# Performance work log

Hardware: AMD Instinct MI355X
Metric: run time of the kernel (lower is better)

## Reference

```python
import jax, jax.numpy as jnp
import numpy as np

B, C, H, W = 2, 128, 96, 96
HEADS, DHEAD, WIN = 4, 32, 5
INNER = HEADS * DHEAD
PAD = WIN // 2


def setup_inputs() -> dict:
    key = jax.random.key(0)
    k1, k2, k3, k4, k5 = jax.random.split(key, 5)
    s = 1.0 / np.sqrt(C)
    return {
        "x": jax.random.normal(k1, (B, C, H, W), dtype=jnp.float32),
        "wq": jax.random.normal(k2, (INNER, C), dtype=jnp.float32) * s,
        "wk": jax.random.normal(k3, (INNER, C), dtype=jnp.float32) * s,
        "wv": jax.random.normal(k4, (INNER, C), dtype=jnp.float32) * s,
        "wproj": jax.random.normal(k5, (C, INNER), dtype=jnp.float32) * s,
    }


def _windows(t):
    # same neighborhood ordering as F.unfold (row-major over kernel offsets).
    tp = jnp.pad(t, ((0, 0), (0, 0), (0, 0), (PAD, PAD), (PAD, PAD)))
    wins = [tp[:, :, :, di:di + H, dj:dj + W]
            for di in range(WIN) for dj in range(WIN)]
    return jnp.stack(wins, axis=3)


def reference(x, wq, wk, wv, wproj):
    # 1x1 convs == per-pixel linear maps
    q = jnp.einsum('oc,bcxy->boxy', wq, x).reshape(B, HEADS, DHEAD, H, W)
    k = jnp.einsum('oc,bcxy->boxy', wk, x).reshape(B, HEADS, DHEAD, H, W)
    v = jnp.einsum('oc,bcxy->boxy', wv, x).reshape(B, HEADS, DHEAD, H, W)

    k_win = _windows(k)  # (B,h,d,25,H,W)
    v_win = _windows(v)

    scale = 1.0 / np.sqrt(DHEAD)
    attn = jnp.einsum('bhdxy,bhdkxy->bhkxy', q, k_win) * scale
    attn = jax.nn.softmax(attn, axis=2)  # softmax over the 25 window positions
    out = jnp.einsum('bhkxy,bhdkxy->bhdxy', attn, v_win)

    out = out.reshape(B, INNER, H, W)
    return jnp.einsum('co,boxy->bcxy', wproj, out)
```

## Files before the change

kernel.cpp:

```cpp
#include <hip/hip_runtime.h>
#include <hip/hip_bf16.h>
#include <hip/hip_fp16.h>

#define PP 9216
#define OO 384

typedef _Float16 f16x8 __attribute__((ext_vector_type(8)));
typedef _Float16 h2    __attribute__((ext_vector_type(2)));
typedef float    f32x4 __attribute__((ext_vector_type(4)));

#if defined(__has_builtin)
# if __has_builtin(__builtin_amdgcn_fdot2)
#  define HAS_FDOT2 1
# endif
#endif

__device__ __forceinline__ float dot2acc(h2 a, h2 b, float c) {
#ifdef HAS_FDOT2
    return __builtin_amdgcn_fdot2(a, b, c, false);
#else
    return c + (float)a[0] * (float)b[0] + (float)a[1] * (float)b[1];
#endif
}

__global__ __launch_bounds__(256) void prep(
    const float* __restrict__ x, const float* __restrict__ wq,
    const float* __restrict__ wk, const float* __restrict__ wv,
    const float* __restrict__ wp,
    _Float16* __restrict__ xT, _Float16* __restrict__ wqkv,
    _Float16* __restrict__ wproj)
{
    const int t = threadIdx.x;
    if (blockIdx.y == 4) {
        if (blockIdx.z) return;
        int idx = blockIdx.x * 256 + t;
        if (idx < 49152) {
            int o = idx >> 7;
            const float* src = (o < 128) ? wq : ((o < 256) ? wk : wv);
            wqkv[idx] = (_Float16)src[(o & 127) * 128 + (idx & 127)];
        } else if (idx < 65536) {
            int j = idx - 49152;
            wproj[j] = (_Float16)wp[j];
        }
        return;
    }
    __shared__ float sT[32][33];
    const int p0 = blockIdx.x * 32;
    const int c0 = blockIdx.y * 32;
    const int b  = blockIdx.z;
    const int row = t >> 3, col = t & 7;

    const float* xb = x + (size_t)b * 128 * PP;
    float4 v = *(const float4*)(xb + (size_t)(c0 + row) * PP + p0 + col * 4);
    sT[col * 4 + 0][row] = v.x;
    sT[col * 4 + 1][row] = v.y;
    sT[col * 4 + 2][row] = v.z;
    sT[col * 4 + 3][row] = v.w;
    __syncthreads();

    _Float16 h[4];
    #pragma unroll
    for (int j = 0; j < 4; j++) h[j] = (_Float16)sT[row][col * 4 + j];
    *(ushort4*)(xT + (size_t)b * PP * 128 + (size_t)(p0 + row) * 128 + c0 + col * 4) =
        *(ushort4*)h;
}

__global__ __launch_bounds__(256) void qkv_gemm(
    const _Float16* __restrict__ xT, const _Float16* __restrict__ wqkv,
    _Float16* __restrict__ qkv)
{
    __shared__ _Float16 sEpi[4][32][104];

    const int b = blockIdx.z;
    const int p0 = blockIdx.x * 64;
    const int nbase = blockIdx.y * 192;
    const int t = threadIdx.x;
    const int w = t >> 6, lane = t & 63;
    const int lm = lane & 15, quad = lane >> 4;
    const int ms0 = (w & 1) * 32;
    const int nw = (w >> 1) * 96;

    const _Float16* xb = xT + (size_t)b * PP * 128;
    _Float16* qb = qkv + (size_t)b * PP * OO;

    f16x8 A[2][4];
    #pragma unroll
    for (int ms = 0; ms < 2; ms++)
        #pragma unroll
        for (int kc = 0; kc < 4; kc++)
            A[ms][kc] = *(const f16x8*)(xb + (size_t)(p0 + ms0 + ms * 16 + lm) * 128
                                        + kc * 32 + quad * 8);

    for (int nt = 0; nt < 6; nt++) {
        const int n0 = nbase + nw + nt * 16;
        f16x8 Bf[4];
        #pragma unroll
        for (int kc = 0; kc < 4; kc++)
            Bf[kc] = *(const f16x8*)(wqkv + (size_t)(n0 + lm) * 128 + kc * 32 + quad * 8);
        f32x4 acc[2];
        #pragma unroll
        for (int ms = 0; ms < 2; ms++) {
            acc[ms] = (f32x4){0.f, 0.f, 0.f, 0.f};
            #pragma unroll
            for (int kc = 0; kc < 4; kc++)
                acc[ms] = __builtin_amdgcn_mfma_f32_16x16x32_f16(A[ms][kc], Bf[kc], acc[ms], 0, 0, 0);
        }
        #pragma unroll
        for (int ms = 0; ms < 2; ms++)
            #pragma unroll
            for (int r = 0; r < 4; r++)
                sEpi[w][ms * 16 + quad * 4 + r][nt * 16 + lm] = (_Float16)acc[ms][r];
    }

    #pragma unroll
    for (int it = 0; it < 6; it++) {
        int idx = it * 64 + lane;
        int row = idx / 12;
        int ch  = idx % 12;
        uint4 v = *(const uint4*)&sEpi[w][row][ch * 8];
        *(uint4*)(qb + (size_t)(p0 + ms0 + row) * OO + nbase + nw + ch * 8) = v;
    }
}

__global__ __launch_bounds__(256) void attn2(
    const _Float16* __restrict__ qkv, _Float16* __restrict__ ao)
{
    __shared__ _Float16 sK[144 * 40];
    __shared__ _Float16 sV[144 * 40];
    __shared__ float sS[64 * 28];

    const int t = threadIdx.x;
    const int x0 = blockIdx.x * 8, y0 = blockIdx.y * 8;
    const int b = blockIdx.z >> 2, h = blockIdx.z & 3;
    const _Float16* base = qkv + (size_t)b * PP * OO;

    for (int u = t; u < 288; u += 256) {
        const int arr = (u >= 144) ? 1 : 0;
        const int pos = u - 144 * arr;
        const int gy = y0 - 2 + pos / 12;
        const int gx = x0 - 2 + pos % 12;
        _Float16* dst = (arr ? sV : sK) + pos * 40;
        if ((unsigned)gy < 96u && (unsigned)gx < 96u) {
            const _Float16* src = base + (size_t)(gy * 96 + gx) * OO + 128 + arr * 128 + h * 32;
            #pragma unroll
            for (int j = 0; j < 4; j++)
                *(uint4*)(dst + j * 8) = *(const uint4*)(src + j * 8);
        } else {
            uint4 z = {0u, 0u, 0u, 0u};
            #pragma unroll
            for (int j = 0; j < 4; j++) *(uint4*)(dst + j * 8) = z;
        }
    }

    const int px = t & 63, w = t >> 6;
    const int ly = px >> 3, lx = px & 7;
    const int gp = (y0 + ly) * 96 + x0 + lx;

    h2 qreg[16];
    {
        const _Float16* qs = base + (size_t)gp * OO + h * 32;
        #pragma unroll
        for (int j = 0; j < 4; j++)
            *(uint4*)(&qreg[j * 4]) = *(const uint4*)(qs + j * 8);
    }
    __syncthreads();

    const float scale = 0.17677669529663689f;
    for (int pos = w; pos < 25; pos += 4) {
        const int hp = (ly + pos / 5) * 12 + lx + pos % 5;
        const _Float16* kr = sK + hp * 40;
        h2 kreg[16];
        #pragma unroll
        for (int j = 0; j < 4; j++)
            *(uint4*)(&kreg[j * 4]) = *(const uint4*)(kr + j * 8);
        float s0 = 0.f, s1 = 0.f;
        #pragma unroll
        for (int j = 0; j < 8; j++) {
            s0 = dot2acc(qreg[2 * j], kreg[2 * j], s0);
            s1 = dot2acc(qreg[2 * j + 1], kreg[2 * j + 1], s1);
        }
        sS[px * 28 + pos] = (s0 + s1) * scale;
    }
    __syncthreads();

    if (t < 64) {
        float* row = sS + t * 28;
        float m = row[0];
        #pragma unroll
        for (int p = 1; p < 25; p++) m = fmaxf(m, row[p]);
        float sum = 0.f;
        float e[25];
        #pragma unroll
        for (int p = 0; p < 25; p++) { e[p] = __expf(row[p] - m); sum += e[p]; }
        const float inv = 1.f / sum;
        #pragma unroll
        for (int p = 0; p < 25; p++) row[p] = e[p] * inv;
    }
    __syncthreads();

    float at[25];
    #pragma unroll
    for (int p = 0; p < 25; p++) at[p] = sS[px * 28 + p];

    float f[8];
    #pragma unroll
    for (int j = 0; j < 8; j++) f[j] = 0.f;
    for (int p = 0; p < 25; p++) {
        const int hp = (ly + p / 5) * 12 + lx + p % 5;
        h2 vreg[4];
        *(uint4*)vreg = *(const uint4*)(sV + hp * 40 + w * 8);
        #pragma unroll
        for (int j = 0; j < 4; j++) {
            f[2 * j]     += at[p] * (float)vreg[j][0];
            f[2 * j + 1] += at[p] * (float)vreg[j][1];
        }
    }
    _Float16 ho[8];
    #pragma unroll
    for (int j = 0; j < 8; j++) ho[j] = (_Float16)f[j];
    *(uint4*)(ao + ((size_t)b * PP + gp) * 128 + h * 32 + w * 8) = *(uint4*)ho;
}

__global__ __launch_bounds__(256) void proj_gemm(
    const _Float16* __restrict__ ao, const _Float16* __restrict__ wproj,
    float* __restrict__ out)
{
    const int b = blockIdx.z;
    const int p0 = blockIdx.x * 64;
    const int t = threadIdx.x;
    const int w = t >> 6, lane = t & 63;
    const int lm = lane & 15, quad = lane >> 4;
    const int ms0 = (w & 1) * 32;
    const int nw = (w >> 1) * 64;

    const _Float16* ab = ao + (size_t)b * PP * 128;
    float* ob = out + (size_t)b * 128 * PP;

    f16x8 A[2][4];
    #pragma unroll
    for (int ms = 0; ms < 2; ms++)
        #pragma unroll
        for (int kc = 0; kc < 4; kc++)
            A[ms][kc] = *(const f16x8*)(ab + (size_t)(p0 + ms0 + ms * 16 + lm) * 128
                                        + kc * 32 + quad * 8);

    for (int nt = 0; nt < 4; nt++) {
        const int n0 = nw + nt * 16;
        f16x8 Bf[4];
        #pragma unroll
        for (int kc = 0; kc < 4; kc++)
            Bf[kc] = *(const f16x8*)(wproj + (size_t)(n0 + lm) * 128 + kc * 32 + quad * 8);
        f32x4 acc[2];
        #pragma unroll
        for (int ms = 0; ms < 2; ms++) {
            acc[ms] = (f32x4){0.f, 0.f, 0.f, 0.f};
            #pragma unroll
            for (int kc = 0; kc < 4; kc++)
                acc[ms] = __builtin_amdgcn_mfma_f32_16x16x32_f16(A[ms][kc], Bf[kc], acc[ms], 0, 0, 0);
        }
        #pragma unroll
        for (int ms = 0; ms < 2; ms++) {
            float4 v = make_float4(acc[ms][0], acc[ms][1], acc[ms][2], acc[ms][3]);
            *(float4*)(ob + (size_t)(n0 + lm) * PP + p0 + ms0 + ms * 16 + quad * 4) = v;
        }
    }
}

extern "C" void kernel_launch(void* const* d_in, const int* in_sizes, int n_in,
                              void* d_out, int out_size, void* d_ws, size_t ws_size,
                              hipStream_t stream)
{
    const float* x  = (const float*)d_in[0];
    const float* wq = (const float*)d_in[1];
    const float* wk = (const float*)d_in[2];
    const float* wv = (const float*)d_in[3];
    const float* wp = (const float*)d_in[4];
    float* out = (float*)d_out;

    _Float16* ws    = (_Float16*)d_ws;
    _Float16* xT    = ws;
    _Float16* wqkv  = xT + 2359296;
    _Float16* wproj = wqkv + 49152;
    _Float16* qkvh  = wproj + 16384;
    _Float16* aoh   = qkvh + 7077888;

    prep<<<dim3(288, 5, 2), 256, 0, stream>>>(x, wq, wk, wv, wp, xT, wqkv, wproj);
    qkv_gemm<<<dim3(144, 2, 2), 256, 0, stream>>>(xT, wqkv, qkvh);
    attn2<<<dim3(12, 12, 8), 256, 0, stream>>>(qkvh, aoh);
    proj_gemm<<<dim3(144, 1, 2), 256, 0, stream>>>(aoh, wproj, out);
}
```

Baseline: 107.6 us.

## Fuse input transpose and weight conversion into QKV and projection GEMMs

Removes the separate prep kernel that transposed x to fp16 and converted the weights. The QKV GEMM now loads fp32 x tiles straight into shared memory, converts them to fp16 when building the A fragments, and reuses that shared buffer for the epilogue. Both GEMMs read fp32 weights directly and convert them in registers. This drops one launch and the xT round trip through global memory. In exchange, each block does more scalar conversion and strided shared-memory reads, and the weights are converted again in every block.

Measured after the change: 114.9 us. +6.8%, slower.

```diff
diff --git a/kernel.cpp b/kernel.cpp
--- a/kernel.cpp
+++ b/kernel.cpp
@@ -23,53 +23,12 @@
 #endif
 }
 
-__global__ __launch_bounds__(256) void prep(
+__global__ __launch_bounds__(256) void qkv_fused(
     const float* __restrict__ x, const float* __restrict__ wq,
     const float* __restrict__ wk, const float* __restrict__ wv,
-    const float* __restrict__ wp,
-    _Float16* __restrict__ xT, _Float16* __restrict__ wqkv,
-    _Float16* __restrict__ wproj)
-{
-    const int t = threadIdx.x;
-    if (blockIdx.y == 4) {
-        if (blockIdx.z) return;
-        int idx = blockIdx.x * 256 + t;
-        if (idx < 49152) {
-            int o = idx >> 7;
-            const float* src = (o < 128) ? wq : ((o < 256) ? wk : wv);
-            wqkv[idx] = (_Float16)src[(o & 127) * 128 + (idx & 127)];
-        } else if (idx < 65536) {
-            int j = idx - 49152;
-            wproj[j] = (_Float16)wp[j];
-        }
-        return;
-    }
-    __shared__ float sT[32][33];
-    const int p0 = blockIdx.x * 32;
-    const int c0 = blockIdx.y * 32;
-    const int b  = blockIdx.z;
-    const int row = t >> 3, col = t & 7;
-
-    const float* xb = x + (size_t)b * 128 * PP;
-    float4 v = *(const float4*)(xb + (size_t)(c0 + row) * PP + p0 + col * 4);
-    sT[col * 4 + 0][row] = v.x;
-    sT[col * 4 + 1][row] = v.y;
-    sT[col * 4 + 2][row] = v.z;
-    sT[col * 4 + 3][row] = v.w;
-    __syncthreads();
-
-    _Float16 h[4];
-    #pragma unroll
-    for (int j = 0; j < 4; j++) h[j] = (_Float16)sT[row][col * 4 + j];
-    *(ushort4*)(xT + (size_t)b * PP * 128 + (size_t)(p0 + row) * 128 + c0 + col * 4) =
-        *(ushort4*)h;
-}
-
-__global__ __launch_bounds__(256) void qkv_gemm(
-    const _Float16* __restrict__ xT, const _Float16* __restrict__ wqkv,
     _Float16* __restrict__ qkv)
 {
-    __shared__ _Float16 sEpi[4][32][104];
+    __shared__ float sX[128 * 70];
 
     const int b = blockIdx.z;
     const int p0 = blockIdx.x * 64;
@@ -80,23 +39,49 @@
     const int ms0 = (w & 1) * 32;
     const int nw = (w >> 1) * 96;
 
-    const _Float16* xb = xT + (size_t)b * PP * 128;
+    const float* xb = x + (size_t)b * 128 * PP;
     _Float16* qb = qkv + (size_t)b * PP * OO;
 
+    #pragma unroll
+    for (int i = 0; i < 8; i++) {
+        int idx = t + 256 * i;
+        int c  = idx >> 4;
+        int p4 = idx & 15;
+        *(float4*)&sX[c * 70 + p4 * 4] =
+            *(const float4*)(xb + (size_t)c * PP + p0 + p4 * 4);
+    }
+    __syncthreads();
+
     f16x8 A[2][4];
     #pragma unroll
-    for (int ms = 0; ms < 2; ms++)
-        #pragma unroll
-        for (int kc = 0; kc < 4; kc++)
-            A[ms][kc] = *(const f16x8*)(xb + (size_t)(p0 + ms0 + ms * 16 + lm) * 128
-                                        + kc * 32 + quad * 8);
+    for (int ms = 0; ms < 2; ms++) {
+        const int px = ms0 + ms * 16 + lm;
+        #pragma unroll
+        for (int kc = 0; kc < 4; kc++) {
+            const int c0 = kc * 32 + quad * 8;
+            f16x8 a;
+            #pragma unroll
+            for (int j = 0; j < 8; j++) a[j] = (_Float16)sX[(c0 + j) * 70 + px];
+            A[ms][kc] = a;
+        }
+    }
+    __syncthreads();
+
+    _Float16* sE = (_Float16*)sX + w * (32 * 104);
 
     for (int nt = 0; nt < 6; nt++) {
-        const int n0 = nbase + nw + nt * 16;
+        const int o0 = nbase + nw + nt * 16 + lm;
+        const float* wsrc = (o0 < 128) ? (wq + (size_t)o0 * 128)
+                          : (o0 < 256) ? (wk + (size_t)(o0 - 128) * 128)
+                                       : (wv + (size_t)(o0 - 256) * 128);
         f16x8 Bf[4];
         #pragma unroll
-        for (int kc = 0; kc < 4; kc++)
-            Bf[kc] = *(const f16x8*)(wqkv + (size_t)(n0 + lm) * 128 + kc * 32 + quad * 8);
+        for (int kc = 0; kc < 4; kc++) {
+            float4 a0 = *(const float4*)(wsrc + kc * 32 + quad * 8);
+            float4 a1 = *(const float4*)(wsrc + kc * 32 + quad * 8 + 4);
+            Bf[kc] = (f16x8){(_Float16)a0.x, (_Float16)a0.y, (_Float16)a0.z, (_Float16)a0.w,
+                             (_Float16)a1.x, (_Float16)a1.y, (_Float16)a1.z, (_Float16)a1.w};
+        }
         f32x4 acc[2];
         #pragma unroll
         for (int ms = 0; ms < 2; ms++) {
@@ -109,7 +94,7 @@
         for (int ms = 0; ms < 2; ms++)
             #pragma unroll
             for (int r = 0; r < 4; r++)
-                sEpi[w][ms * 16 + quad * 4 + r][nt * 16 + lm] = (_Float16)acc[ms][r];
+                sE[(ms * 16 + quad * 4 + r) * 104 + nt * 16 + lm] = (_Float16)acc[ms][r];
     }
 
     #pragma unroll
@@ -117,7 +102,7 @@
         int idx = it * 64 + lane;
         int row = idx / 12;
         int ch  = idx % 12;
-        uint4 v = *(const uint4*)&sEpi[w][row][ch * 8];
+        uint4 v = *(const uint4*)(sE + row * 104 + ch * 8);
         *(uint4*)(qb + (size_t)(p0 + ms0 + row) * OO + nbase + nw + ch * 8) = v;
     }
 }
@@ -222,7 +207,7 @@
 }
 
 __global__ __launch_bounds__(256) void proj_gemm(
-    const _Float16* __restrict__ ao, const _Float16* __restrict__ wproj,
+    const _Float16* __restrict__ ao, const float* __restrict__ wp,
     float* __restrict__ out)
 {
     const int b = blockIdx.z;
@@ -246,10 +231,15 @@
 
     for (int nt = 0; nt < 4; nt++) {
         const int n0 = nw + nt * 16;
+        const float* wsrc = wp + (size_t)(n0 + lm) * 128;
         f16x8 Bf[4];
         #pragma unroll
-        for (int kc = 0; kc < 4; kc++)
-            Bf[kc] = *(const f16x8*)(wproj + (size_t)(n0 + lm) * 128 + kc * 32 + quad * 8);
+        for (int kc = 0; kc < 4; kc++) {
+            float4 a0 = *(const float4*)(wsrc + kc * 32 + quad * 8);
+            float4 a1 = *(const float4*)(wsrc + kc * 32 + quad * 8 + 4);
+            Bf[kc] = (f16x8){(_Float16)a0.x, (_Float16)a0.y, (_Float16)a0.z, (_Float16)a0.w,
+                             (_Float16)a1.x, (_Float16)a1.y, (_Float16)a1.z, (_Float16)a1.w};
+        }
         f32x4 acc[2];
         #pragma unroll
         for (int ms = 0; ms < 2; ms++) {
@@ -277,15 +267,11 @@
     const float* wp = (const float*)d_in[4];
     float* out = (float*)d_out;
 
-    _Float16* ws    = (_Float16*)d_ws;
-    _Float16* xT    = ws;
-    _Float16* wqkv  = xT + 2359296;
-    _Float16* wproj = wqkv + 49152;
-    _Float16* qkvh  = wproj + 16384;
-    _Float16* aoh   = qkvh + 7077888;
-
-    prep<<<dim3(288, 5, 2), 256, 0, stream>>>(x, wq, wk, wv, wp, xT, wqkv, wproj);
-    qkv_gemm<<<dim3(144, 2, 2), 256, 0, stream>>>(xT, wqkv, qkvh);
+    _Float16* ws   = (_Float16*)d_ws;
+    _Float16* qkvh = ws;
+    _Float16* aoh  = qkvh + 7077888;
+
+    qkv_fused<<<dim3(144, 2, 2), 256, 0, stream>>>(x, wq, wk, wv, qkvh);
     attn2<<<dim3(12, 12, 8), 256, 0, stream>>>(qkvh, aoh);
-    proj_gemm<<<dim3(144, 1, 2), 256, 0, stream>>>(aoh, wproj, out);
-}
+    proj_gemm<<<dim3(144, 1, 2), 256, 0, stream>>>(aoh, wp, out);
+}
```
